# Performance work log

Hardware: AMD Instinct MI355X
Metric: run time of the kernel (lower is better)

## Reference

```python
import jax, jax.numpy as jnp
import numpy as np

N, IN_F, OUT_F = 65536, 512, 512


def setup_inputs() -> dict:
    key = jax.random.key(0)
    k1, k2, k3 = jax.random.split(key, 3)
    # Activations arrive as dequant-pending uint8-valued floats in [0, 256).
    x = jax.random.randint(k1, (N, IN_F), 0, 256).astype(jnp.float32)
    weight = jax.random.randint(k2, (OUT_F, IN_F), 0, 256).astype(jnp.int32)
    bias = jax.random.randint(k3, (OUT_F,), -512, 512).astype(jnp.int32)
    return {
        "x": x,
        "weight": weight,
        "bias": bias,
        "M": jnp.asarray(0.0123, dtype=jnp.float32),
        "x_zero": jnp.asarray(128.0, dtype=jnp.float32),
        "w_zero": jnp.asarray(128.0, dtype=jnp.float32),
        "y_zero": jnp.asarray(128.0, dtype=jnp.float32),
    }


def reference(x, weight, bias, M, x_zero, w_zero, y_zero):
    # y = round(linear(x - x_zero, w - w_zero, b) * M + y_zero)
    xs = x - x_zero                                   # [N, IN_F]
    w = weight.astype(jnp.float32) - w_zero           # [OUT_F, IN_F]
    y = jnp.einsum("ni,oi->no", xs, w) + bias.astype(jnp.float32)
    return jnp.round(y * M + y_zero)
```

## Files before the change

kernel.cpp:

```cpp
#include <hip/hip_runtime.h>


#define K_DIM 512
#define OUTF  512
#define BM    128
#define BN    128
#define BK    64
#define NT    8
#define LDAB  80
#define TILE_B (128 * LDAB)
#define BUF_B  (2 * TILE_B)

typedef __attribute__((ext_vector_type(4))) int i32x4;
typedef __attribute__((ext_vector_type(4))) float f32x4;

__device__ __forceinline__ unsigned int pack4(float a, float b, float c, float d, float z) {
    unsigned int b0 = (unsigned int)((int)(a - z)) & 0xffu;
    unsigned int b1 = (unsigned int)((int)(b - z)) & 0xffu;
    unsigned int b2 = (unsigned int)((int)(c - z)) & 0xffu;
    unsigned int b3 = (unsigned int)((int)(d - z)) & 0xffu;
    return b0 | (b1 << 8) | (b2 << 16) | (b3 << 24);
}

__global__ void wprep(const int* __restrict__ W, unsigned int* __restrict__ Wb,
                      const float* __restrict__ wzp) {
    float wz = wzp[0];
    int idx = (blockIdx.x * blockDim.x + threadIdx.x) * 4;
    i32x4 w = *reinterpret_cast<const i32x4*>(W + idx);
    Wb[idx >> 2] = pack4((float)w[0], (float)w[1], (float)w[2], (float)w[3], wz);
}

__global__ __launch_bounds__(512, 4)
void qgemm(const float* __restrict__ X,
           const unsigned char* __restrict__ Wb,
           const int* __restrict__ bias,
           const float* __restrict__ Mp,
           const float* __restrict__ xzp,
           const float* __restrict__ yzp,
           float* __restrict__ Y) {
    __shared__ unsigned char lds[2 * BUF_B];

    const int tid  = threadIdx.x;
    const int lane = tid & 63;
    const int wid  = tid >> 6;
    const int wr   = wid >> 2;
    const int wc   = wid & 3;
    const int fr   = lane & 15;
    const int fq   = lane >> 4;

    const int b = blockIdx.x;
    const int lid = (b & 7) * 256 + (b >> 3);
    const int row0 = (lid >> 2) * BM;
    const int n0   = (lid & 3) * BN;

    const float xz = xzp[0];

    const int srow = tid >> 2;
    const int scol = (tid & 3) * 16;
    const float* xbase = X + (size_t)(row0 + srow) * K_DIM + scol;
    const unsigned char* wbase = Wb + (size_t)(n0 + srow) * K_DIM + scol;
    const int aoff = srow * LDAB + scol;
    const int boff = TILE_B + srow * LDAB + scol;

    f32x4 ra[4];
    i32x4 rb;

    auto stage = [&](int t) {
        const float* xp = xbase + t * BK;
        #pragma unroll
        for (int q = 0; q < 4; ++q)
            ra[q] = *reinterpret_cast<const f32x4*>(xp + q * 4);
        rb = *reinterpret_cast<const i32x4*>(wbase + t * BK);
    };
    auto convwrite = [&](int buf) {
        const int ab = buf * BUF_B;
        i32x4 pa;
        #pragma unroll
        for (int q = 0; q < 4; ++q)
            pa[q] = (int)pack4(ra[q][0], ra[q][1], ra[q][2], ra[q][3], xz);
        *reinterpret_cast<i32x4*>(&lds[ab + aoff]) = pa;
        *reinterpret_cast<i32x4*>(&lds[ab + boff]) = rb;
    };

    i32x4 acc[4][2] = {};

    const int aro = (wr * 64 + fr) * LDAB + fq * 16;
    const int bro = TILE_B + (wc * 32 + fr) * LDAB + fq * 16;

    auto compute = [&](int buf) {
        const int ab = buf * BUF_B;
        i32x4 af[4], bf[2];
        #pragma unroll
        for (int m = 0; m < 4; ++m)
            af[m] = *reinterpret_cast<const i32x4*>(&lds[ab + aro + m * 16 * LDAB]);
        #pragma unroll
        for (int n = 0; n < 2; ++n)
            bf[n] = *reinterpret_cast<const i32x4*>(&lds[ab + bro + n * 16 * LDAB]);
        #pragma unroll
        for (int m = 0; m < 4; ++m)
            #pragma unroll
            for (int n = 0; n < 2; ++n)
                acc[m][n] = __builtin_amdgcn_mfma_i32_16x16x64_i8(
                    af[m], bf[n], acc[m][n], 0, 0, 0);
    };

    stage(0);
    convwrite(0);
    __syncthreads();

    #pragma unroll
    for (int t = 0; t < NT; ++t) {
        if (t < NT - 1) stage(t + 1);
        compute(t & 1);
        if (t < NT - 1) convwrite((t + 1) & 1);
        __syncthreads();
    }

    const float M = Mp[0], yz = yzp[0];
    #pragma unroll
    for (int n = 0; n < 2; ++n) {
        const int col = n0 + wc * 32 + n * 16 + fr;
        const int bv = bias[col];
        #pragma unroll
        for (int m = 0; m < 4; ++m) {
            const int row = row0 + wr * 64 + m * 16 + fq * 4;
            float* yp = Y + (size_t)row * OUTF + col;
            #pragma unroll
            for (int j = 0; j < 4; ++j)
                yp[(size_t)j * OUTF] = rintf((float)(acc[m][n][j] + bv) * M + yz);
        }
    }
}

extern "C" void kernel_launch(void* const* d_in, const int* in_sizes, int n_in,
                              void* d_out, int out_size, void* d_ws, size_t ws_size,
                              hipStream_t stream) {
    const float* x    = (const float*)d_in[0];
    const int*   w    = (const int*)d_in[1];
    const int*   bias = (const int*)d_in[2];
    const float* M    = (const float*)d_in[3];
    const float* xz   = (const float*)d_in[4];
    const float* wz   = (const float*)d_in[5];
    const float* yz   = (const float*)d_in[6];
    float* y = (float*)d_out;
    unsigned int* Wb = (unsigned int*)d_ws;

    wprep<<<256, 256, 0, stream>>>(w, Wb, wz);
    qgemm<<<2048, 512, 0, stream>>>(x, (const unsigned char*)Wb, bias, M, xz, yz, y);
}
```

Measured before the change: 76.54 us.

## Pre-quantize X to int8 in a separate pass and stream via global_load_lds

Adds an xprep kernel that converts the fp32 activations to packed int8 in workspace once. The GEMM then reads the 4x smaller int8 tiles directly into LDS with global_load_lds, and uses a 256-thread block where each wave computes a 4x4 grid of 16x16 MFMA tiles. The aim is to remove the repeated fp32 loads and per-tile conversion work from the GEMM's inner pipeline. In exchange it adds a full extra pass over X (read fp32, write int8) plus a kernel launch, and it keeps a fallback kernel for when the workspace is too small.

```diff
diff --git a/kernel.cpp b/kernel.cpp
--- a/kernel.cpp
+++ b/kernel.cpp
@@ -3,41 +3,142 @@
 
 #define K_DIM 512
 #define OUTF  512
-#define BM    128
-#define BN    128
-#define BK    64
 #define NT    8
+
+typedef __attribute__((ext_vector_type(4))) int i32x4;
+typedef __attribute__((ext_vector_type(4))) float f32x4;
+typedef __attribute__((ext_vector_type(4))) unsigned int u32x4;
+
+__device__ __forceinline__ void gload16(const void* g, void* l) {
+    __builtin_amdgcn_global_load_lds(
+        (const __attribute__((address_space(1))) void*)g,
+        (__attribute__((address_space(3))) void*)l,
+        16, 0, 0);
+}
+
+__global__ void wprep(const int* __restrict__ W, unsigned int* __restrict__ Wb,
+                      const float* __restrict__ wzp) {
+    const int wz = __float2int_rn(wzp[0]);
+    int idx = (blockIdx.x * blockDim.x + threadIdx.x) * 4;
+    i32x4 w = *reinterpret_cast<const i32x4*>(W + idx);
+    unsigned int b0 = (unsigned int)(w[0] - wz) & 0xffu;
+    unsigned int b1 = (unsigned int)(w[1] - wz) & 0xffu;
+    unsigned int b2 = (unsigned int)(w[2] - wz) & 0xffu;
+    unsigned int b3 = (unsigned int)(w[3] - wz) & 0xffu;
+    Wb[idx >> 2] = b0 | (b1 << 8) | (b2 << 16) | (b3 << 24);
+}
+
+__global__ __launch_bounds__(256)
+void xprep(const float* __restrict__ X, u32x4* __restrict__ Xb,
+           const float* __restrict__ xzp) {
+    const int xz = __float2int_rn(xzp[0]);
+    size_t i = (size_t)blockIdx.x * blockDim.x + threadIdx.x;
+    const f32x4* xp = reinterpret_cast<const f32x4*>(X) + i * 4;
+    u32x4 o;
+    #pragma unroll
+    for (int q = 0; q < 4; ++q) {
+        f32x4 v = xp[q];
+        unsigned int b0 = (unsigned int)((int)v[0] - xz) & 0xffu;
+        unsigned int b1 = (unsigned int)((int)v[1] - xz) & 0xffu;
+        unsigned int b2 = (unsigned int)((int)v[2] - xz) & 0xffu;
+        unsigned int b3 = (unsigned int)((int)v[3] - xz) & 0xffu;
+        o[q] = b0 | (b1 << 8) | (b2 << 16) | (b3 << 24);
+    }
+    Xb[i] = o;
+}
+
+__global__ __launch_bounds__(256, 4)
+void qgemm(const unsigned char* __restrict__ Xb,
+           const unsigned char* __restrict__ Wb,
+           const int* __restrict__ bias,
+           const float* __restrict__ Mp,
+           const float* __restrict__ yzp,
+           float* __restrict__ Y) {
+    __shared__ unsigned char lds[2][16384];
+
+    const int tid  = threadIdx.x;
+    const int lane = tid & 63;
+    const int wid  = tid >> 6;
+    const int wr   = wid >> 1;
+    const int wc   = wid & 1;
+    const int fr   = lane & 15;
+    const int fq   = lane >> 4;
+
+    const int b = blockIdx.x;
+    const int lid = (b & 7) * 256 + (b >> 3);
+    const int row0 = (lid >> 2) * 128;
+    const int n0   = (lid & 3) * 128;
+
+    const unsigned char* gA = Xb + (size_t)(row0 + wid * 32 + fr) * K_DIM + fq * 16;
+    const unsigned char* gB = Wb + (size_t)(n0   + wid * 32 + fr) * K_DIM + fq * 16;
+    const int ldsA = wid * 2048;
+    const int ldsB = 8192 + wid * 2048;
+
+    i32x4 acc[4][4] = {};
+
+    auto stage = [&](int t, int buf) {
+        const unsigned char* ga = gA + t * 64;
+        const unsigned char* gb = gB + t * 64;
+        gload16(ga,              &lds[buf][ldsA]);
+        gload16(ga + 16 * K_DIM, &lds[buf][ldsA + 1024]);
+        gload16(gb,              &lds[buf][ldsB]);
+        gload16(gb + 16 * K_DIM, &lds[buf][ldsB + 1024]);
+    };
+
+    auto compute = [&](int buf) {
+        i32x4 af[4], bf[4];
+        #pragma unroll
+        for (int m = 0; m < 4; ++m)
+            af[m] = *reinterpret_cast<const i32x4*>(&lds[buf][(wr * 4 + m) * 1024 + lane * 16]);
+        #pragma unroll
+        for (int n = 0; n < 4; ++n)
+            bf[n] = *reinterpret_cast<const i32x4*>(&lds[buf][8192 + (wc * 4 + n) * 1024 + lane * 16]);
+        #pragma unroll
+        for (int m = 0; m < 4; ++m)
+            #pragma unroll
+            for (int n = 0; n < 4; ++n)
+                acc[m][n] = __builtin_amdgcn_mfma_i32_16x16x64_i8(
+                    af[m], bf[n], acc[m][n], 0, 0, 0);
+    };
+
+    stage(0, 0);
+    __syncthreads();
+
+    #pragma unroll
+    for (int t = 0; t < NT; ++t) {
+        if (t < NT - 1) stage(t + 1, (t + 1) & 1);
+        compute(t & 1);
+        __syncthreads();
+    }
+
+    const float M = Mp[0], yz = yzp[0];
+    #pragma unroll
+    for (int n = 0; n < 4; ++n) {
+        const int col = n0 + wc * 64 + n * 16 + fr;
+        const int bv = bias[col];
+        #pragma unroll
+        for (int m = 0; m < 4; ++m) {
+            const int row = row0 + wr * 64 + m * 16 + fq * 4;
+            float* yp = Y + (size_t)row * OUTF + col;
+            #pragma unroll
+            for (int j = 0; j < 4; ++j)
+                yp[(size_t)j * OUTF] = rintf((float)(acc[m][n][j] + bv) * M + yz);
+        }
+    }
+}
+
 #define LDAB  80
 #define TILE_B (128 * LDAB)
 #define BUF_B  (2 * TILE_B)
 
-typedef __attribute__((ext_vector_type(4))) int i32x4;
-typedef __attribute__((ext_vector_type(4))) float f32x4;
-
-__device__ __forceinline__ unsigned int pack4(float a, float b, float c, float d, float z) {
-    unsigned int b0 = (unsigned int)((int)(a - z)) & 0xffu;
-    unsigned int b1 = (unsigned int)((int)(b - z)) & 0xffu;
-    unsigned int b2 = (unsigned int)((int)(c - z)) & 0xffu;
-    unsigned int b3 = (unsigned int)((int)(d - z)) & 0xffu;
-    return b0 | (b1 << 8) | (b2 << 16) | (b3 << 24);
-}
-
-__global__ void wprep(const int* __restrict__ W, unsigned int* __restrict__ Wb,
-                      const float* __restrict__ wzp) {
-    float wz = wzp[0];
-    int idx = (blockIdx.x * blockDim.x + threadIdx.x) * 4;
-    i32x4 w = *reinterpret_cast<const i32x4*>(W + idx);
-    Wb[idx >> 2] = pack4((float)w[0], (float)w[1], (float)w[2], (float)w[3], wz);
-}
-
 __global__ __launch_bounds__(512, 4)
-void qgemm(const float* __restrict__ X,
-           const unsigned char* __restrict__ Wb,
-           const int* __restrict__ bias,
-           const float* __restrict__ Mp,
-           const float* __restrict__ xzp,
-           const float* __restrict__ yzp,
-           float* __restrict__ Y) {
+void qgemm_fb(const float* __restrict__ X,
+              const unsigned char* __restrict__ Wb,
+              const int* __restrict__ bias,
+              const float* __restrict__ Mp,
+              const float* __restrict__ xzp,
+              const float* __restrict__ yzp,
+              float* __restrict__ Y) {
     __shared__ unsigned char lds[2 * BUF_B];
 
     const int tid  = threadIdx.x;
@@ -50,10 +151,10 @@
 
     const int b = blockIdx.x;
     const int lid = (b & 7) * 256 + (b >> 3);
-    const int row0 = (lid >> 2) * BM;
-    const int n0   = (lid & 3) * BN;
-
-    const float xz = xzp[0];
+    const int row0 = (lid >> 2) * 128;
+    const int n0   = (lid & 3) * 128;
+
+    const int xz = __float2int_rn(xzp[0]);
 
     const int srow = tid >> 2;
     const int scol = (tid & 3) * 16;
@@ -66,24 +167,28 @@
     i32x4 rb;
 
     auto stage = [&](int t) {
-        const float* xp = xbase + t * BK;
+        const float* xp = xbase + t * 64;
         #pragma unroll
         for (int q = 0; q < 4; ++q)
             ra[q] = *reinterpret_cast<const f32x4*>(xp + q * 4);
-        rb = *reinterpret_cast<const i32x4*>(wbase + t * BK);
+        rb = *reinterpret_cast<const i32x4*>(wbase + t * 64);
     };
     auto convwrite = [&](int buf) {
         const int ab = buf * BUF_B;
         i32x4 pa;
         #pragma unroll
-        for (int q = 0; q < 4; ++q)
-            pa[q] = (int)pack4(ra[q][0], ra[q][1], ra[q][2], ra[q][3], xz);
+        for (int q = 0; q < 4; ++q) {
+            unsigned int b0 = (unsigned int)((int)ra[q][0] - xz) & 0xffu;
+            unsigned int b1 = (unsigned int)((int)ra[q][1] - xz) & 0xffu;
+            unsigned int b2 = (unsigned int)((int)ra[q][2] - xz) & 0xffu;
+            unsigned int b3 = (unsigned int)((int)ra[q][3] - xz) & 0xffu;
+            pa[q] = (int)(b0 | (b1 << 8) | (b2 << 16) | (b3 << 24));
+        }
         *reinterpret_cast<i32x4*>(&lds[ab + aoff]) = pa;
         *reinterpret_cast<i32x4*>(&lds[ab + boff]) = rb;
     };
 
     i32x4 acc[4][2] = {};
-
     const int aro = (wr * 64 + fr) * LDAB + fq * 16;
     const int bro = TILE_B + (wc * 32 + fr) * LDAB + fq * 16;
 
@@ -143,8 +248,17 @@
     const float* wz   = (const float*)d_in[5];
     const float* yz   = (const float*)d_in[6];
     float* y = (float*)d_out;
-    unsigned int* Wb = (unsigned int*)d_ws;
-
-    wprep<<<256, 256, 0, stream>>>(w, Wb, wz);
-    qgemm<<<2048, 512, 0, stream>>>(x, (const unsigned char*)Wb, bias, M, xz, yz, y);
-}
+
+    unsigned char* Wb = (unsigned char*)d_ws;
+    unsigned char* Xbp = Wb + 256 * 1024;
+    const size_t need = 256 * 1024 + (size_t)65536 * 512;
+
+    wprep<<<256, 256, 0, stream>>>(w, (unsigned int*)Wb, wz);
+
+    if (ws_size >= need) {
+        xprep<<<8192, 256, 0, stream>>>(x, (u32x4*)Xbp, xz);
+        qgemm<<<2048, 256, 0, stream>>>(Xbp, Wb, bias, M, yz, y);
+    } else {
+        qgemm_fb<<<2048, 512, 0, stream>>>(x, Wb, bias, M, xz, yz, y);
+    }
+}
```

New measurement: 88.79 us. 16.0% more time.

## Keep weight fragments in registers and stream X directly without LDS

Applied to the files above, without the earlier changes.

Drops LDS staging entirely. Each wave holds a 32-column slice of the int8 weights in registers for the full K, then walks 16 row tiles in a persistent loop. X is loaded straight into MFMA fragment layout with register double-buffered prefetch. Bias is folded into the accumulator init, which removes the LDS traffic and barriers. In exchange, each wave now loads X on its own (four waves per block read the same rows, so reuse depends on cache), and the bf arrays add register pressure.

```diff
diff --git a/kernel.cpp b/kernel.cpp
--- a/kernel.cpp
+++ b/kernel.cpp
@@ -3,34 +3,23 @@
 
 #define K_DIM 512
 #define OUTF  512
-#define BM    128
-#define BN    128
-#define BK    64
-#define NT    8
-#define LDAB  80
-#define TILE_B (128 * LDAB)
-#define BUF_B  (2 * TILE_B)
 
-typedef __attribute__((ext_vector_type(4))) int i32x4;
+typedef __attribute__((ext_vector_type(4))) int   i32x4;
 typedef __attribute__((ext_vector_type(4))) float f32x4;
-
-__device__ __forceinline__ unsigned int pack4(float a, float b, float c, float d, float z) {
-    unsigned int b0 = (unsigned int)((int)(a - z)) & 0xffu;
-    unsigned int b1 = (unsigned int)((int)(b - z)) & 0xffu;
-    unsigned int b2 = (unsigned int)((int)(c - z)) & 0xffu;
-    unsigned int b3 = (unsigned int)((int)(d - z)) & 0xffu;
-    return b0 | (b1 << 8) | (b2 << 16) | (b3 << 24);
-}
 
 __global__ void wprep(const int* __restrict__ W, unsigned int* __restrict__ Wb,
                       const float* __restrict__ wzp) {
-    float wz = wzp[0];
+    const int wz = __float2int_rn(wzp[0]);
     int idx = (blockIdx.x * blockDim.x + threadIdx.x) * 4;
     i32x4 w = *reinterpret_cast<const i32x4*>(W + idx);
-    Wb[idx >> 2] = pack4((float)w[0], (float)w[1], (float)w[2], (float)w[3], wz);
+    unsigned int p = ((unsigned int)(w[0] - wz) & 0xffu)
+                   | (((unsigned int)(w[1] - wz) & 0xffu) << 8)
+                   | (((unsigned int)(w[2] - wz) & 0xffu) << 16)
+                   | (((unsigned int)(w[3] - wz) & 0xffu) << 24);
+    Wb[idx >> 2] = p;
 }
 
-__global__ __launch_bounds__(512, 4)
+__global__ __launch_bounds__(256, 4)
 void qgemm(const float* __restrict__ X,
            const unsigned char* __restrict__ Wb,
            const int* __restrict__ bias,
@@ -38,97 +27,86 @@
            const float* __restrict__ xzp,
            const float* __restrict__ yzp,
            float* __restrict__ Y) {
-    __shared__ unsigned char lds[2 * BUF_B];
-
     const int tid  = threadIdx.x;
     const int lane = tid & 63;
     const int wid  = tid >> 6;
-    const int wr   = wid >> 2;
-    const int wc   = wid & 3;
     const int fr   = lane & 15;
     const int fq   = lane >> 4;
 
-    const int b = blockIdx.x;
-    const int lid = (b & 7) * 256 + (b >> 3);
-    const int row0 = (lid >> 2) * BM;
-    const int n0   = (lid & 3) * BN;
+    const int b    = blockIdx.x;
+    const int q    = b >> 3;
+    const int c    = q & 3;
+    const int rbase= (b & 7) * 32 + (q >> 2);
 
-    const float xz = xzp[0];
+    const int c0 = c * 128 + wid * 32;
 
-    const int srow = tid >> 2;
-    const int scol = (tid & 3) * 16;
-    const float* xbase = X + (size_t)(row0 + srow) * K_DIM + scol;
-    const unsigned char* wbase = Wb + (size_t)(n0 + srow) * K_DIM + scol;
-    const int aoff = srow * LDAB + scol;
-    const int boff = TILE_B + srow * LDAB + scol;
+    const float Mv  = Mp[0];
+    const float xzf = xzp[0];
+    const float yzf = yzp[0];
 
-    f32x4 ra[4];
-    i32x4 rb;
+    i32x4 bf0[8], bf1[8];
+    {
+        const unsigned char* wb = Wb + (size_t)(c0 + fr) * K_DIM + fq * 16;
+        #pragma unroll
+        for (int ks = 0; ks < 8; ++ks) {
+            bf0[ks] = *reinterpret_cast<const i32x4*>(wb + ks * 64);
+            bf1[ks] = *reinterpret_cast<const i32x4*>(wb + 16 * K_DIM + ks * 64);
+        }
+    }
 
-    auto stage = [&](int t) {
-        const float* xp = xbase + t * BK;
+    const int bv0 = bias[c0 + fr];
+    const int bv1 = bias[c0 + 16 + fr];
+    const i32x4 init0 = {bv0, bv0, bv0, bv0};
+    const i32x4 init1 = {bv1, bv1, bv1, bv1};
+    i32x4 acc0 = init0, acc1 = init1;
+
+    const size_t TILE_STRIDE = (size_t)256 * 16 * K_DIM;
+    const float* ax = X + ((size_t)rbase * 16 + fr) * K_DIM + fq * 16;
+
+    f32x4 bufA[4], bufB[4];
+
+    auto loadA = [&](f32x4 (&dst)[4], const float* p) {
         #pragma unroll
-        for (int q = 0; q < 4; ++q)
-            ra[q] = *reinterpret_cast<const f32x4*>(xp + q * 4);
-        rb = *reinterpret_cast<const i32x4*>(wbase + t * BK);
+        for (int qq = 0; qq < 4; ++qq)
+            dst[qq] = *reinterpret_cast<const f32x4*>(p + qq * 4);
     };
-    auto convwrite = [&](int buf) {
-        const int ab = buf * BUF_B;
-        i32x4 pa;
+    auto convA = [&](const f32x4 (&src)[4], i32x4& af) {
         #pragma unroll
-        for (int q = 0; q < 4; ++q)
-            pa[q] = (int)pack4(ra[q][0], ra[q][1], ra[q][2], ra[q][3], xz);
-        *reinterpret_cast<i32x4*>(&lds[ab + aoff]) = pa;
-        *reinterpret_cast<i32x4*>(&lds[ab + boff]) = rb;
+        for (int qq = 0; qq < 4; ++qq) {
+            unsigned int u0 = (unsigned int)(int)(src[qq][0] - xzf) & 0xffu;
+            unsigned int u1 = (unsigned int)(int)(src[qq][1] - xzf) & 0xffu;
+            unsigned int u2 = (unsigned int)(int)(src[qq][2] - xzf) & 0xffu;
+            unsigned int u3 = (unsigned int)(int)(src[qq][3] - xzf) & 0xffu;
+            af[qq] = (int)(u0 | (u1 << 8) | (u2 << 16) | (u3 << 24));
+        }
     };
 
-    i32x4 acc[4][2] = {};
+    loadA(bufA, ax);
 
-    const int aro = (wr * 64 + fr) * LDAB + fq * 16;
-    const int bro = TILE_B + (wc * 32 + fr) * LDAB + fq * 16;
+    for (int t = 0; t < 16; ++t) {
+        const float* axn = ax + TILE_STRIDE;
+        const float* pfTile = (t < 15) ? axn : ax;
 
-    auto compute = [&](int buf) {
-        const int ab = buf * BUF_B;
-        i32x4 af[4], bf[2];
         #pragma unroll
-        for (int m = 0; m < 4; ++m)
-            af[m] = *reinterpret_cast<const i32x4*>(&lds[ab + aro + m * 16 * LDAB]);
+        for (int ks = 0; ks < 8; ++ks) {
+            const float* pf = (ks < 7) ? (ax + (ks + 1) * 64) : pfTile;
+            i32x4 af;
+            if ((ks & 1) == 0) { loadA(bufB, pf); convA(bufA, af); }
+            else               { loadA(bufA, pf); convA(bufB, af); }
+            acc0 = __builtin_amdgcn_mfma_i32_16x16x64_i8(af, bf0[ks], acc0, 0, 0, 0);
+            acc1 = __builtin_amdgcn_mfma_i32_16x16x64_i8(af, bf1[ks], acc1, 0, 0, 0);
+        }
+
+        const size_t row0t = ((size_t)rbase + (size_t)t * 256) * 16;
+        float* yp = Y + (row0t + fq * 4) * OUTF + c0 + fr;
         #pragma unroll
-        for (int n = 0; n < 2; ++n)
-            bf[n] = *reinterpret_cast<const i32x4*>(&lds[ab + bro + n * 16 * LDAB]);
-        #pragma unroll
-        for (int m = 0; m < 4; ++m)
-            #pragma unroll
-            for (int n = 0; n < 2; ++n)
-                acc[m][n] = __builtin_amdgcn_mfma_i32_16x16x64_i8(
-                    af[m], bf[n], acc[m][n], 0, 0, 0);
-    };
-
-    stage(0);
-    convwrite(0);
-    __syncthreads();
-
-    #pragma unroll
-    for (int t = 0; t < NT; ++t) {
-        if (t < NT - 1) stage(t + 1);
-        compute(t & 1);
-        if (t < NT - 1) convwrite((t + 1) & 1);
-        __syncthreads();
-    }
-
-    const float M = Mp[0], yz = yzp[0];
-    #pragma unroll
-    for (int n = 0; n < 2; ++n) {
-        const int col = n0 + wc * 32 + n * 16 + fr;
-        const int bv = bias[col];
-        #pragma unroll
-        for (int m = 0; m < 4; ++m) {
-            const int row = row0 + wr * 64 + m * 16 + fq * 4;
-            float* yp = Y + (size_t)row * OUTF + col;
-            #pragma unroll
-            for (int j = 0; j < 4; ++j)
-                yp[(size_t)j * OUTF] = rintf((float)(acc[m][n][j] + bv) * M + yz);
+        for (int j = 0; j < 4; ++j) {
+            yp[(size_t)j * OUTF]      = rintf((float)acc0[j] * Mv + yzf);
+            yp[(size_t)j * OUTF + 16] = rintf((float)acc1[j] * Mv + yzf);
         }
+        acc0 = init0;
+        acc1 = init1;
+        ax = axn;
     }
 }
 
@@ -143,8 +121,9 @@
     const float* wz   = (const float*)d_in[5];
     const float* yz   = (const float*)d_in[6];
     float* y = (float*)d_out;
+
     unsigned int* Wb = (unsigned int*)d_ws;
 
     wprep<<<256, 256, 0, stream>>>(w, Wb, wz);
-    qgemm<<<2048, 512, 0, stream>>>(x, (const unsigned char*)Wb, bias, M, xz, yz, y);
+    qgemm<<<1024, 256, 0, stream>>>(x, (const unsigned char*)Wb, bias, M, xz, yz, y);
 }
```

Result: slower. 249.5 us (+226.0%).
